# Optimization experiments

Hardware: AMD Instinct MI355X
Metric: run time of the kernel (lower is better)

## Reference

```python
import jax, jax.numpy as jnp
import numpy as np

IN, H, OUT, T = 512, 2048, 512, 8192


def setup_inputs() -> dict:
    key = jax.random.key(0)
    ks = jax.random.split(key, 9)
    s = 1.0 / np.sqrt(H).astype(np.float32)  # PyTorch LSTM/Linear init range
    u = lambda k, shape: jax.random.uniform(k, shape, jnp.float32, -s, s)
    return {
        "sequence": jax.random.normal(ks[0], (T, IN), jnp.float32),
        "W_ih": u(ks[1], (4 * H, IN)),
        "W_hh": u(ks[2], (4 * H, H)),
        "b_ih": u(ks[3], (4 * H,)),
        "b_hh": u(ks[4], (4 * H,)),
        "h0": jax.random.normal(ks[5], (H,), jnp.float32),  # module's random hidden init (batch=1 flattened)
        "c0": jax.random.normal(ks[6], (H,), jnp.float32),
        "W_lin": u(ks[7], (OUT, H)),
        "b_lin": u(ks[8], (OUT,)),
    }


def reference(sequence, W_ih, W_hh, b_ih, b_hh, h0, c0, W_lin, b_lin):
    # Precompute input contribution to gates for all timesteps in one GEMM: [T, 4H]
    x_gates = sequence @ W_ih.T + (b_ih + b_hh)

    def cell(carry, xg):
        h, c = carry
        g = xg + h @ W_hh.T                      # [4H]
        i, f, gg, o = jnp.split(g, 4)            # PyTorch gate order: i, f, g, o
        i = jax.nn.sigmoid(i)
        f = jax.nn.sigmoid(f)
        gg = jnp.tanh(gg)
        o = jax.nn.sigmoid(o)
        c = f * c + i * gg
        h = o * jnp.tanh(c)
        return (h, c), h

    (h_last, _), _ = jax.lax.scan(cell, (h0, c0), x_gates)
    # linear on every step then take last == linear on last hidden state
    pred = h_last @ W_lin.T + b_lin              # [OUT]
    return pred[None, :]                          # [1, OUT], matches prediction[-1]
```

## Files before the change

kernel.cpp:

```cpp
#include <hip/hip_runtime.h>
#include <hip/hip_bf16.h>
#include <stdint.h>



__device__ __forceinline__ uint32_t packbf(float a, float b) {
    uint32_t ua = __float_as_uint(a);
    uint32_t ub = __float_as_uint(b);
    ua = (ua + 0x7fffu + ((ua >> 16) & 1u)) >> 16;
    ub = (ub + 0x7fffu + ((ub >> 16) & 1u)) >> 16;
    return ua | (ub << 16);
}

__device__ __forceinline__ float dot2bf(uint32_t a, uint32_t b, float c) {
    float d;
    asm("v_dot2_f32_bf16 %0, %1, %2, %3" : "=v"(d) : "v"(a), "v"(b), "v"(c));
    return d;
}

__device__ __forceinline__ float sigm(float x) { return 1.f / (1.f + __expf(-x)); }
__device__ __forceinline__ float tanh_fast(float x) { return 1.f - 2.f / (1.f + __expf(2.f * x)); }

#define ASTORE(p, v) __hip_atomic_store((p), (v), __ATOMIC_RELAXED, __HIP_MEMORY_SCOPE_AGENT)

__device__ __forceinline__ void aload_2x4(const unsigned long long* pa,
                                          const unsigned long long* pb,
                                          ulonglong2& ra, ulonglong2& rb) {
    asm volatile(
        "global_load_dwordx4 %0, %2, off sc0 sc1\n\t"
        "global_load_dwordx4 %1, %3, off sc0 sc1\n\t"
        "s_waitcnt vmcnt(0)"
        : "=v"(ra), "=v"(rb)
        : "v"(pa), "v"(pb)
        : "memory");
}

__global__ __launch_bounds__(256) void init_hbuf(unsigned long long* hbuf) {
    int i = blockIdx.x * 256 + threadIdx.x;
    if (i < 2048) hbuf[i] = ~0ull;
}

__global__ __launch_bounds__(256, 1) void lstm_persist(const float* __restrict__ seq,
                                                       const float* __restrict__ Wih,
                                                       const float* __restrict__ Whh,
                                                       const float* __restrict__ bih,
                                                       const float* __restrict__ bhh,
                                                       const float* __restrict__ h0,
                                                       const float* __restrict__ c0,
                                                       unsigned long long* hbuf,
                                                       float* __restrict__ hf32) {
    const int b = blockIdx.x, tid = threadIdx.x;
    const int q = tid >> 6, lane = tid & 63;
    const int hb = b * 8;
    const int rb = (lane >> 2) & 1;
    const int myrow = hb + 2 * q + rb;

    uint32_t w[160];
#pragma unroll
    for (int c = 0; c < 8; c++) {
        const int R = (c >> 1) * 2048 + hb + 2 * q + (c & 1);
        const float2* rih = (const float2*)(Wih + (size_t)R * 512);
        const float2* rhh = (const float2*)(Whh + (size_t)R * 2048);
#pragma unroll
        for (int k = 0; k < 4; k++) {
            float2 v = rih[k * 64 + lane];
            w[c * 20 + k] = packbf(v.x, v.y);
        }
#pragma unroll
        for (int k = 4; k < 20; k++) {
            float2 v = rhh[(k - 4) * 64 + lane];
            w[c * 20 + k] = packbf(v.x, v.y);
        }
    }

    __shared__ uint32_t v_stage[2][1024];

    const float bi  = bih[myrow] + bhh[myrow];
    const float bf_ = bih[2048 + myrow] + bhh[2048 + myrow];
    const float bg  = bih[4096 + myrow] + bhh[4096 + myrow];
    const float bo  = bih[6144 + myrow] + bhh[6144 + myrow];
    float c_state = c0[myrow];

    if (q == 0 && lane < 4) {
        float a = h0[hb + lane * 2], b2 = h0[hb + lane * 2 + 1];
        unsigned long long v = ((unsigned long long)packbf(a, b2) << 32);
        ASTORE(&hbuf[b * 4 + lane], v);
    }

    float2 xn[4];
#pragma unroll
    for (int k = 0; k < 4; k++) xn[k] = ((const float2*)seq)[k * 64 + lane];

    int gave_up = 0;

    for (int s = 1; s <= 8192; s++) {
        const int t = s - 1, bs = t & 1;
        const uint32_t want = (uint32_t)t;

        float acc[8];
        {
            uint32_t x0 = packbf(xn[0].x, xn[0].y), x1 = packbf(xn[1].x, xn[1].y);
            uint32_t x2 = packbf(xn[2].x, xn[2].y), x3 = packbf(xn[3].x, xn[3].y);
#pragma unroll
            for (int c = 0; c < 8; c++) {
                float a0 = dot2bf(w[c * 20 + 0], x0, 0.f);
                a0 = dot2bf(w[c * 20 + 1], x1, a0);
                a0 = dot2bf(w[c * 20 + 2], x2, a0);
                acc[c] = dot2bf(w[c * 20 + 3], x3, a0);
            }
        }

        {
            const unsigned long long* base = hbuf + (bs << 10) + q * 256;
            const unsigned long long* pa = base + 2 * lane;
            const unsigned long long* pb = base + 128 + 2 * lane;
            ulonglong2 ra, rb2;
            if (!gave_up) {
                int tries = 0;
                for (;;) {
                    aload_2x4(pa, pb, ra, rb2);
                    int ok = ((uint32_t)ra.x == want) & ((uint32_t)ra.y == want) &
                             ((uint32_t)rb2.x == want) & ((uint32_t)rb2.y == want);
                    if (__all(ok)) break;
                    if (++tries > (1 << 17)) { gave_up = 1; break; }
                    if (tries > 2) __builtin_amdgcn_s_sleep(1);
                }
            } else {
                aload_2x4(pa, pb, ra, rb2);
            }
            uint2* vsa = (uint2*)&v_stage[bs][q * 256 + 2 * lane];
            uint2* vsb = (uint2*)&v_stage[bs][q * 256 + 128 + 2 * lane];
            *vsa = make_uint2((uint32_t)(ra.x >> 32), (uint32_t)(ra.y >> 32));
            *vsb = make_uint2((uint32_t)(rb2.x >> 32), (uint32_t)(rb2.y >> 32));
        }

        if (s < 8192) {
            const float2* xp = (const float2*)(seq + (size_t)s * 512);
#pragma unroll
            for (int k = 0; k < 4; k++) xn[k] = xp[k * 64 + lane];
        }

        __syncthreads();

#pragma unroll
        for (int k = 0; k < 16; k++) {
            uint32_t hv = v_stage[bs][k * 64 + lane];
#pragma unroll
            for (int c = 0; c < 8; c++) acc[c] = dot2bf(w[c * 20 + 4 + k], hv, acc[c]);
        }

#pragma unroll
        for (int j = 0; j < 4; j++) {
            float lo = acc[j], hi = acc[j + 4];
            float sel = (lane & 1) ? lo : hi;
            float got = __shfl_xor(sel, 1, 64);
            acc[j] = ((lane & 1) ? hi : lo) + got;
        }
#pragma unroll
        for (int j = 0; j < 2; j++) {
            float lo = acc[j], hi = acc[j + 2];
            float sel = (lane & 2) ? lo : hi;
            float got = __shfl_xor(sel, 2, 64);
            acc[j] = ((lane & 2) ? hi : lo) + got;
        }
        {
            float lo = acc[0], hi = acc[1];
            float sel = (lane & 4) ? lo : hi;
            float got = __shfl_xor(sel, 4, 64);
            acc[0] = ((lane & 4) ? hi : lo) + got;
        }
        acc[0] += __shfl_xor(acc[0], 8, 64);
        acc[0] += __shfl_xor(acc[0], 16, 64);
        acc[0] += __shfl_xor(acc[0], 32, 64);

        const int base = lane & ~3;
        float gi = __shfl(acc[0], base, 64);
        float gg = __shfl(acc[0], base + 1, 64);
        float gf = __shfl(acc[0], base + 2, 64);
        float go = __shfl(acc[0], base + 3, 64);
        float i_ = sigm(gi + bi), f_ = sigm(gf + bf_), g_ = tanh_fast(gg + bg), o_ = sigm(go + bo);
        c_state = f_ * c_state + i_ * g_;
        float hval = o_ * tanh_fast(c_state);

        float h1 = __shfl(hval, 4, 64);
        if (lane == 0) {
            unsigned long long v = ((unsigned long long)packbf(hval, h1) << 32) | (uint32_t)s;
            ASTORE(&hbuf[((s & 1) << 10) + b * 4 + q], v);
            if (s == 8192) { hf32[hb + 2 * q] = hval; hf32[hb + 2 * q + 1] = h1; }
        }
    }
}

__global__ __launch_bounds__(256) void final_linear(const float* __restrict__ hf,
                                                    const float* __restrict__ Wlin,
                                                    const float* __restrict__ blin,
                                                    float* __restrict__ out) {
    const int row = blockIdx.x * 4 + (threadIdx.x >> 6);
    const int lane = threadIdx.x & 63;
    float acc = 0.f;
#pragma unroll
    for (int it = 0; it < 8; it++) {
        int c = it * 256 + lane * 4;
        float4 wv = *(const float4*)&Wlin[(size_t)row * 2048 + c];
        float4 hv = *(const float4*)&hf[c];
        acc += wv.x * hv.x + wv.y * hv.y + wv.z * hv.z + wv.w * hv.w;
    }
#pragma unroll
    for (int off = 32; off; off >>= 1) acc += __shfl_xor(acc, off, 64);
    if (lane == 0) out[row] = acc + blin[row];
}

extern "C" void kernel_launch(void* const* d_in, const int* in_sizes, int n_in,
                              void* d_out, int out_size, void* d_ws, size_t ws_size,
                              hipStream_t stream) {
    const float* seq  = (const float*)d_in[0];
    const float* Wih  = (const float*)d_in[1];
    const float* Whh  = (const float*)d_in[2];
    const float* bih  = (const float*)d_in[3];
    const float* bhh  = (const float*)d_in[4];
    const float* h0   = (const float*)d_in[5];
    const float* c0   = (const float*)d_in[6];
    const float* Wlin = (const float*)d_in[7];
    const float* blin = (const float*)d_in[8];
    float* out = (float*)d_out;

    char* ws = (char*)d_ws;
    unsigned long long* hbuf = (unsigned long long*)ws;
    float* hf32 = (float*)(ws + 16384);

    init_hbuf<<<8, 256, 0, stream>>>(hbuf);
    lstm_persist<<<256, 256, 0, stream>>>(seq, Wih, Whh, bih, bhh, h0, c0, hbuf, hf32);
    final_linear<<<128, 256, 0, stream>>>(hf32, Wlin, blin, out);
}
```

Before: 15.96 ms.

## Replace per-step block barrier with per-wave LDS flags and overlap h polling

Removes the __syncthreads in the recurrent loop. Each wave now publishes a step-tagged flag in shared memory after staging its slice of h, and consumers spin on the per-quarter flags with acquire loads, consuming each quarter as soon as it is ready. The global h loads are issued as relaxed atomics before the input-projection dot products so their latency overlaps that work. The W_hh register layout is reshuffled so each lane reads 16-byte vectors from LDS. The cost is more fragile intra-block synchronisation that relies on explicit lgkmcnt waits and spin loops.

```diff
diff --git a/kernel.cpp b/kernel.cpp
--- a/kernel.cpp
+++ b/kernel.cpp
@@ -22,18 +22,9 @@
 __device__ __forceinline__ float tanh_fast(float x) { return 1.f - 2.f / (1.f + __expf(2.f * x)); }
 
 #define ASTORE(p, v) __hip_atomic_store((p), (v), __ATOMIC_RELAXED, __HIP_MEMORY_SCOPE_AGENT)
-
-__device__ __forceinline__ void aload_2x4(const unsigned long long* pa,
-                                          const unsigned long long* pb,
-                                          ulonglong2& ra, ulonglong2& rb) {
-    asm volatile(
-        "global_load_dwordx4 %0, %2, off sc0 sc1\n\t"
-        "global_load_dwordx4 %1, %3, off sc0 sc1\n\t"
-        "s_waitcnt vmcnt(0)"
-        : "=v"(ra), "=v"(rb)
-        : "v"(pa), "v"(pb)
-        : "memory");
-}
+#define ALOAD(p)     __hip_atomic_load((p), __ATOMIC_RELAXED, __HIP_MEMORY_SCOPE_AGENT)
+#define LDS_ST(p, v) __hip_atomic_store((p), (v), __ATOMIC_RELAXED, __HIP_MEMORY_SCOPE_WORKGROUP)
+#define LDS_LDACQ(p) __hip_atomic_load((p), __ATOMIC_ACQUIRE, __HIP_MEMORY_SCOPE_WORKGROUP)
 
 __global__ __launch_bounds__(256) void init_hbuf(unsigned long long* hbuf) {
     int i = blockIdx.x * 256 + threadIdx.x;
@@ -67,13 +58,17 @@
             w[c * 20 + k] = packbf(v.x, v.y);
         }
 #pragma unroll
-        for (int k = 4; k < 20; k++) {
-            float2 v = rhh[(k - 4) * 64 + lane];
-            w[c * 20 + k] = packbf(v.x, v.y);
-        }
-    }
-
-    __shared__ uint32_t v_stage[2][1024];
+        for (int j = 0; j < 4; j++)
+#pragma unroll
+            for (int i = 0; i < 4; i++) {
+                float2 v = rhh[256 * j + 4 * lane + i];
+                w[c * 20 + 4 + 4 * j + i] = packbf(v.x, v.y);
+            }
+    }
+
+    __shared__ alignas(16) uint32_t v_stage[2][1024];
+    __shared__ alignas(16) uint32_t qflag[2][4];
+    if (tid < 8) ((uint32_t*)qflag)[tid] = 0;
 
     const float bi  = bih[myrow] + bhh[myrow];
     const float bf_ = bih[2048 + myrow] + bhh[2048 + myrow];
@@ -91,47 +86,52 @@
 #pragma unroll
     for (int k = 0; k < 4; k++) xn[k] = ((const float2*)seq)[k * 64 + lane];
 
+    __syncthreads();
+
     int gave_up = 0;
 
     for (int s = 1; s <= 8192; s++) {
         const int t = s - 1, bs = t & 1;
         const uint32_t want = (uint32_t)t;
 
+        uint32_t x0 = packbf(xn[0].x, xn[0].y), x1 = packbf(xn[1].x, xn[1].y);
+        uint32_t x2 = packbf(xn[2].x, xn[2].y), x3 = packbf(xn[3].x, xn[3].y);
+
+        const unsigned long long* base = hbuf + (bs << 10) + q * 256;
+        const unsigned long long* pa = base + 2 * lane;
+        const unsigned long long* pb = base + 128 + 2 * lane;
+        unsigned long long a0 = ALOAD(pa), a1 = ALOAD(pa + 1);
+        unsigned long long b0 = ALOAD(pb), b1 = ALOAD(pb + 1);
+
         float acc[8];
+#pragma unroll
+        for (int c = 0; c < 8; c++) {
+            float a = dot2bf(w[c * 20 + 0], x0, 0.f);
+            a = dot2bf(w[c * 20 + 1], x1, a);
+            a = dot2bf(w[c * 20 + 2], x2, a);
+            acc[c] = dot2bf(w[c * 20 + 3], x3, a);
+        }
+
+        if (!gave_up) {
+            int tries = 0;
+            for (;;) {
+                int ok = ((uint32_t)a0 == want) & ((uint32_t)a1 == want) &
+                         ((uint32_t)b0 == want) & ((uint32_t)b1 == want);
+                if (__all(ok)) break;
+                if (++tries > (1 << 17)) { gave_up = 1; break; }
+                if (tries > 2) __builtin_amdgcn_s_sleep(1);
+                a0 = ALOAD(pa); a1 = ALOAD(pa + 1);
+                b0 = ALOAD(pb); b1 = ALOAD(pb + 1);
+            }
+        }
+
         {
-            uint32_t x0 = packbf(xn[0].x, xn[0].y), x1 = packbf(xn[1].x, xn[1].y);
-            uint32_t x2 = packbf(xn[2].x, xn[2].y), x3 = packbf(xn[3].x, xn[3].y);
-#pragma unroll
-            for (int c = 0; c < 8; c++) {
-                float a0 = dot2bf(w[c * 20 + 0], x0, 0.f);
-                a0 = dot2bf(w[c * 20 + 1], x1, a0);
-                a0 = dot2bf(w[c * 20 + 2], x2, a0);
-                acc[c] = dot2bf(w[c * 20 + 3], x3, a0);
-            }
-        }
-
-        {
-            const unsigned long long* base = hbuf + (bs << 10) + q * 256;
-            const unsigned long long* pa = base + 2 * lane;
-            const unsigned long long* pb = base + 128 + 2 * lane;
-            ulonglong2 ra, rb2;
-            if (!gave_up) {
-                int tries = 0;
-                for (;;) {
-                    aload_2x4(pa, pb, ra, rb2);
-                    int ok = ((uint32_t)ra.x == want) & ((uint32_t)ra.y == want) &
-                             ((uint32_t)rb2.x == want) & ((uint32_t)rb2.y == want);
-                    if (__all(ok)) break;
-                    if (++tries > (1 << 17)) { gave_up = 1; break; }
-                    if (tries > 2) __builtin_amdgcn_s_sleep(1);
-                }
-            } else {
-                aload_2x4(pa, pb, ra, rb2);
-            }
             uint2* vsa = (uint2*)&v_stage[bs][q * 256 + 2 * lane];
             uint2* vsb = (uint2*)&v_stage[bs][q * 256 + 128 + 2 * lane];
-            *vsa = make_uint2((uint32_t)(ra.x >> 32), (uint32_t)(ra.y >> 32));
-            *vsb = make_uint2((uint32_t)(rb2.x >> 32), (uint32_t)(rb2.y >> 32));
+            *vsa = make_uint2((uint32_t)(a0 >> 32), (uint32_t)(a1 >> 32));
+            *vsb = make_uint2((uint32_t)(b0 >> 32), (uint32_t)(b1 >> 32));
+            asm volatile("s_waitcnt lgkmcnt(0)" ::: "memory");
+            if (lane == 0) LDS_ST(&qflag[bs][q], (uint32_t)s);
         }
 
         if (s < 8192) {
@@ -140,13 +140,22 @@
             for (int k = 0; k < 4; k++) xn[k] = xp[k * 64 + lane];
         }
 
-        __syncthreads();
-
-#pragma unroll
-        for (int k = 0; k < 16; k++) {
-            uint32_t hv = v_stage[bs][k * 64 + lane];
-#pragma unroll
-            for (int c = 0; c < 8; c++) acc[c] = dot2bf(w[c * 20 + 4 + k], hv, acc[c]);
+        const uint32_t su = (uint32_t)s;
+#pragma unroll
+        for (int j = 0; j < 4; j++) {
+            uint32_t fj = LDS_LDACQ(&qflag[bs][j]);
+            if (fj != su) {
+                int zz = 0;
+                do { fj = LDS_LDACQ(&qflag[bs][j]); } while (fj != su && ++zz < (1 << 20));
+            }
+            const uint4 hv = *(const uint4*)&v_stage[bs][256 * j + 4 * lane];
+#pragma unroll
+            for (int c = 0; c < 8; c++) {
+                float a = dot2bf(w[c * 20 + 4 + 4 * j + 0], hv.x, acc[c]);
+                a = dot2bf(w[c * 20 + 4 + 4 * j + 1], hv.y, a);
+                a = dot2bf(w[c * 20 + 4 + 4 * j + 2], hv.z, a);
+                acc[c] = dot2bf(w[c * 20 + 4 + 4 * j + 3], hv.w, a);
+            }
         }
 
 #pragma unroll
@@ -173,11 +182,11 @@
         acc[0] += __shfl_xor(acc[0], 16, 64);
         acc[0] += __shfl_xor(acc[0], 32, 64);
 
-        const int base = lane & ~3;
-        float gi = __shfl(acc[0], base, 64);
-        float gg = __shfl(acc[0], base + 1, 64);
-        float gf = __shfl(acc[0], base + 2, 64);
-        float go = __shfl(acc[0], base + 3, 64);
+        const int base2 = lane & ~3;
+        float gi = __shfl(acc[0], base2, 64);
+        float gg = __shfl(acc[0], base2 + 1, 64);
+        float gf = __shfl(acc[0], base2 + 2, 64);
+        float go = __shfl(acc[0], base2 + 3, 64);
         float i_ = sigm(gi + bi), f_ = sigm(gf + bf_), g_ = tanh_fast(gg + bg), o_ = sigm(go + bo);
         c_state = f_ * c_state + i_ * g_;
         float hval = o_ * tanh_fast(c_state);
```

Result: slower. 43.68 ms (+173.7%).
